# Kernel optimization log

Measured on AMD Instinct MI355X. Metric: run time of the kernel, lower is better.

Reference implementation:

```python
import jax, jax.numpy as jnp
import numpy as np

B = 1
S = 256          # sequence_size (pair repr is S x S)
C = 128          # channel_size_pair
NHEAD = 4
HID = 32         # hidden_channel
SCALE = 1.0 / float(np.sqrt(HID))
EPS = 1e-5


def setup_inputs() -> dict:
    key = jax.random.key(0)
    ks = jax.random.split(key, 9)
    init = 0.02
    return {
        "pair_repr": jax.random.normal(ks[0], (B, S, S, C), dtype=jnp.float32),
        "gamma": jnp.ones((C,), dtype=jnp.float32),
        "beta": jnp.zeros((C,), dtype=jnp.float32),
        "Wq": jax.random.normal(ks[1], (C, NHEAD * HID), dtype=jnp.float32) * init,
        "Wk": jax.random.normal(ks[2], (C, NHEAD * HID), dtype=jnp.float32) * init,
        "Wv": jax.random.normal(ks[3], (C, NHEAD * HID), dtype=jnp.float32) * init,
        "Wb": jax.random.normal(ks[4], (C, NHEAD), dtype=jnp.float32) * init,
        "Wg": jax.random.normal(ks[5], (C, NHEAD * HID), dtype=jnp.float32) * init,
        "bg": jnp.zeros((NHEAD * HID,), dtype=jnp.float32),
        "Wo": jax.random.normal(ks[6], (NHEAD * HID, C), dtype=jnp.float32) * init,
        "bo": jnp.zeros((C,), dtype=jnp.float32),
    }


def _to_heads(t):
    # [b, h, w, n*d] -> [b, n, h, w, d]
    b, h, w, _ = t.shape
    return t.reshape(b, h, w, NHEAD, HID).transpose(0, 3, 1, 2, 4)


def reference(pair_repr, gamma, beta, Wq, Wk, Wv, Wb, Wg, bg, Wo, bo):
    # LayerNorm over channel dim
    mu = jnp.mean(pair_repr, axis=-1, keepdims=True)
    var = jnp.var(pair_repr, axis=-1, keepdims=True)
    z = (pair_repr - mu) * jax.lax.rsqrt(var + EPS) * gamma + beta

    q = _to_heads(z @ Wq)  # [b, n, i, j, d]
    k = _to_heads(z @ Wk)
    v = _to_heads(z @ Wv)
    g = _to_heads(jax.nn.sigmoid(z @ Wg + bg))

    # bias: [b, h, w, n] -> [b, n, h, w]; 'ending' broadcasts it over the j axis
    bias = (z @ Wb).transpose(0, 3, 1, 2)

    # 'ending' branch: attend over the row index k for each column j
    dots = SCALE * jnp.einsum('bnijd,bnkjd->bnijk', q, k) + bias[:, :, :, None, :]
    attn = jax.nn.softmax(dots, axis=4)
    out = g * jnp.einsum('bnijk,bnkjd->bnijd', attn, v)

    # [b, n, i, j, d] -> [b, i, j, n*d]
    out = out.transpose(0, 2, 3, 1, 4).reshape(B, S, S, NHEAD * HID)
    return out @ Wo + bo
```

## Files before the change

kernel.cpp:

```cpp
#include <hip/hip_runtime.h>
#include <hip/hip_bf16.h>
#include <math.h>

#define SCALE 0.1767766952966369f
#define LN_EPS 1e-5f

typedef short bf16x8 __attribute__((ext_vector_type(8)));
typedef float f32x4 __attribute__((ext_vector_type(4)));

__device__ __forceinline__ unsigned short f2bf(float f) {
    __hip_bfloat16 h = __float2bfloat16(f);
    return *reinterpret_cast<unsigned short*>(&h);
}
__device__ __forceinline__ float bf2f(unsigned short u) {
    union { unsigned int u32; float f; } c;
    c.u32 = ((unsigned int)u) << 16;
    return c.f;
}
__device__ __forceinline__ unsigned int pack2(float a, float b) {
    return (unsigned int)f2bf(a) | ((unsigned int)f2bf(b) << 16);
}

__global__ __launch_bounds__(256)
void k_prep(const float* __restrict__ Wq, const float* __restrict__ Wk,
            const float* __restrict__ Wv, const float* __restrict__ Wg,
            const float* __restrict__ Wo, const float* __restrict__ Wb,
            unsigned short* __restrict__ WT, unsigned short* __restrict__ WbT)
{
    if (blockIdx.x == 20) {
        int t = threadIdx.x;
        int row = t >> 4, k0 = (t & 15) * 8;
        unsigned int u[4];
        #pragma unroll
        for (int e = 0; e < 4; ++e) {
            float a = 0.f, b = 0.f;
            if (row < 4) {
                a = Wb[(k0 + 2*e    )*4 + row];
                b = Wb[(k0 + 2*e + 1)*4 + row];
            }
            u[e] = pack2(a, b);
        }
        *(uint4*)(WbT + row*128 + k0) = make_uint4(u[0], u[1], u[2], u[3]);
        return;
    }
    int idx = blockIdx.x * 256 + threadIdx.x;
    int m   = idx >> 10;
    int col = (idx >> 3) & 127;
    int k0  = (idx & 7) * 16;
    const float* W = (m==0) ? Wq : (m==1) ? Wk : (m==2) ? Wv : (m==3) ? Wg : Wo;
    unsigned int u[8];
    #pragma unroll
    for (int e = 0; e < 8; ++e) {
        float a = W[(k0 + 2*e    )*128 + col];
        float b = W[(k0 + 2*e + 1)*128 + col];
        u[e] = pack2(a, b);
    }
    uint4* dst = (uint4*)(WT + m*16384 + col*128 + k0);
    dst[0] = make_uint4(u[0], u[1], u[2], u[3]);
    dst[1] = make_uint4(u[4], u[5], u[6], u[7]);
}

__global__ __launch_bounds__(256)
void k_ln_proj(const float* __restrict__ x, const float* __restrict__ gamma,
               const float* __restrict__ beta,
               const unsigned short* __restrict__ WT,
               const unsigned short* __restrict__ WbT,
               const float* __restrict__ bg,
               unsigned short* __restrict__ Q, unsigned short* __restrict__ K,
               unsigned short* __restrict__ VT, unsigned short* __restrict__ G,
               float* __restrict__ BIAS)
{
    __shared__ unsigned short Wbuf[64*136];
    __shared__ unsigned short stg[4][2176];

    const int t    = threadIdx.x;
    const int lane = t & 63, w = t >> 6;
    const int l15  = lane & 15, quad = lane >> 4;
    const int j    = blockIdx.x >> 2;
    const int ti   = (blockIdx.x & 3) * 64 + w*16;
    unsigned short* sw = stg[w];

    float v[32];
    {
        const float* xr = x + ((size_t)(ti + l15)*256 + j)*128;
        float sum = 0.f, ssq = 0.f;
        #pragma unroll
        for (int kt = 0; kt < 4; ++kt) {
            float4 f0 = *(const float4*)(xr + kt*32 + quad*8);
            float4 f1 = *(const float4*)(xr + kt*32 + quad*8 + 4);
            v[kt*8+0]=f0.x; v[kt*8+1]=f0.y; v[kt*8+2]=f0.z; v[kt*8+3]=f0.w;
            v[kt*8+4]=f1.x; v[kt*8+5]=f1.y; v[kt*8+6]=f1.z; v[kt*8+7]=f1.w;
            sum += f0.x+f0.y+f0.z+f0.w + f1.x+f1.y+f1.z+f1.w;
            ssq += f0.x*f0.x+f0.y*f0.y+f0.z*f0.z+f0.w*f0.w
                 + f1.x*f1.x+f1.y*f1.y+f1.z*f1.z+f1.w*f1.w;
        }
        sum += __shfl_xor(sum, 16); ssq += __shfl_xor(ssq, 16);
        sum += __shfl_xor(sum, 32); ssq += __shfl_xor(ssq, 32);
        float mu  = sum * (1.f/128.f);
        float var = ssq * (1.f/128.f) - mu*mu;
        float rs  = rsqrtf(var + LN_EPS);
        #pragma unroll
        for (int kt = 0; kt < 4; ++kt)
            #pragma unroll
            for (int e = 0; e < 8; ++e) {
                int c = kt*32 + quad*8 + e;
                v[kt*8+e] = (v[kt*8+e]-mu)*rs*gamma[c] + beta[c];
            }
    }
    bf16x8 afrag[4];
    #pragma unroll
    for (int kt = 0; kt < 4; ++kt)
        #pragma unroll
        for (int e = 0; e < 8; ++e)
            afrag[kt][e] = (short)f2bf(v[kt*8+e]);

    {
        f32x4 bacc = (f32x4){0.f,0.f,0.f,0.f};
        #pragma unroll
        for (int kt = 0; kt < 4; ++kt) {
            bf16x8 b = *(const bf16x8*)(WbT + (size_t)l15*128 + kt*32 + quad*8);
            bacc = __builtin_amdgcn_mfma_f32_16x16x32_bf16(afrag[kt], b, bacc, 0, 0, 0);
        }
        if (l15 < 4) {
            #pragma unroll
            for (int reg = 0; reg < 4; ++reg)
                BIAS[l15*65536 + ((ti >> 2) + quad)*1024 + j*4 + reg] = bacc[reg];
        }
    }

    #pragma unroll 1
    for (int mm = 0; mm < 4; ++mm) {
        f32x4 acc[8];
        #pragma unroll
        for (int nt = 0; nt < 8; ++nt) acc[nt] = (f32x4){0.f,0.f,0.f,0.f};

        #pragma unroll 1
        for (int half = 0; half < 2; ++half) {
            __syncthreads();
            #pragma unroll
            for (int r = 0; r < 4; ++r) {
                int idx = r*256 + t;
                int col = idx >> 4, kc = idx & 15;
                *(uint4*)&Wbuf[col*136 + kc*8] =
                    *(const uint4*)&WT[mm*16384 + (half*64 + col)*128 + kc*8];
            }
            __syncthreads();

            #pragma unroll
            for (int kt = 0; kt < 4; ++kt) {
                #pragma unroll
                for (int nt2 = 0; nt2 < 4; ++nt2) {
                    bf16x8 b = *(const bf16x8*)&Wbuf[(nt2*16 + l15)*136 + kt*32 + quad*8];
                    if (mm == 2)
                        acc[half*4 + nt2] = __builtin_amdgcn_mfma_f32_16x16x32_bf16(
                            b, afrag[kt], acc[half*4 + nt2], 0, 0, 0);
                    else
                        acc[half*4 + nt2] = __builtin_amdgcn_mfma_f32_16x16x32_bf16(
                            afrag[kt], b, acc[half*4 + nt2], 0, 0, 0);
                }
            }
        }

        if (mm == 2) {
            #pragma unroll
            for (int nt = 0; nt < 8; ++nt)
                #pragma unroll
                for (int reg = 0; reg < 4; ++reg)
                    sw[(nt*16 + quad*4 + reg)*16 + l15] = f2bf(acc[nt][reg]);
            #pragma unroll
            for (int it = 0; it < 4; ++it) {
                int idx = it*64 + lane;
                int ch = idx >> 1, c = idx & 1;
                uint4 val = *(const uint4*)&sw[ch*16 + c*8];
                int nh = ch >> 5, d = ch & 31;
                *(uint4*)&VT[(((size_t)(nh*256 + j))*32 + d)*256 + ti + c*8] = val;
            }
        } else {
            #pragma unroll
            for (int nt = 0; nt < 8; ++nt) {
                int cc = nt*16 + l15;
                float bgv = (mm == 3) ? bg[cc] : 0.f;
                #pragma unroll
                for (int reg = 0; reg < 4; ++reg) {
                    float val = acc[nt][reg];
                    if (mm == 0)      val *= SCALE;
                    else if (mm == 3) val = 1.f/(1.f + __expf(-(val + bgv)));
                    sw[(quad*4 + reg)*136 + cc] = f2bf(val);
                }
            }
            {
                int row = lane >> 2, c = lane & 3;
                unsigned short* Dst = (mm == 0) ? Q : (mm == 1) ? K : G;
                #pragma unroll
                for (int nh = 0; nh < 4; ++nh) {
                    uint4 val = *(const uint4*)&sw[row*136 + nh*32 + c*8];
                    *(uint4*)&Dst[(((size_t)(nh*256 + j))*256 + ti + row)*32 + c*8] = val;
                }
            }
        }
    }
}

__global__ __launch_bounds__(256)
void k_attn(const unsigned short* __restrict__ Q, const unsigned short* __restrict__ K,
            const unsigned short* __restrict__ VT, const unsigned short* __restrict__ G,
            const float* __restrict__ BIAS, unsigned short* __restrict__ AO)
{
    __shared__ unsigned short P_lds[4][16*264];

    const int t    = threadIdx.x;
    const int n    = blockIdx.x >> 10;
    const int j    = (blockIdx.x >> 2) & 255;
    const int ic   = blockIdx.x & 3;
    const int lane = t & 63, w = t >> 6;
    const int l15  = lane & 15, quad = lane >> 4;
    const int i0   = ic*64 + w*16;

    const size_t nb = (size_t)(n*256 + j);
    const unsigned short* qb  = Q  + nb*8192;
    const unsigned short* kb  = K  + nb*8192;
    const unsigned short* vtb = VT + nb*8192;
    const unsigned short* gb  = G  + nb*8192;
    const float* biasn = BIAS + n*65536;
    unsigned short* Pw = P_lds[w];

    bf16x8 a = *(const bf16x8*)(qb + (size_t)(i0 + l15)*32 + quad*8);
    f32x4 acc[16];
    #pragma unroll
    for (int kt = 0; kt < 16; ++kt) {
        bf16x8 b = *(const bf16x8*)(kb + (size_t)(kt*16 + l15)*32 + quad*8);
        acc[kt] = __builtin_amdgcn_mfma_f32_16x16x32_bf16(a, b, (f32x4){0.f,0.f,0.f,0.f}, 0, 0, 0);
    }

    float mx[4] = {-1e30f, -1e30f, -1e30f, -1e30f};
    #pragma unroll
    for (int kt = 0; kt < 16; ++kt) {
        float4 bv = *(const float4*)&biasn[((i0 >> 2) + quad)*1024 + (kt*16 + l15)*4];
        acc[kt][0] += bv.x; acc[kt][1] += bv.y;
        acc[kt][2] += bv.z; acc[kt][3] += bv.w;
        #pragma unroll
        for (int reg = 0; reg < 4; ++reg)
            mx[reg] = fmaxf(mx[reg], acc[kt][reg]);
    }
    #pragma unroll
    for (int m = 1; m <= 8; m <<= 1) {
        #pragma unroll
        for (int reg = 0; reg < 4; ++reg)
            mx[reg] = fmaxf(mx[reg], __shfl_xor(mx[reg], m));
    }

    float sm[4] = {0.f, 0.f, 0.f, 0.f};
    #pragma unroll
    for (int kt = 0; kt < 16; ++kt) {
        #pragma unroll
        for (int reg = 0; reg < 4; ++reg) {
            float e = __expf(acc[kt][reg] - mx[reg]);
            acc[kt][reg] = e;
            sm[reg] += e;
        }
    }
    #pragma unroll
    for (int m = 1; m <= 8; m <<= 1) {
        #pragma unroll
        for (int reg = 0; reg < 4; ++reg)
            sm[reg] += __shfl_xor(sm[reg], m);
    }
    float rinv[4];
    #pragma unroll
    for (int reg = 0; reg < 4; ++reg) rinv[reg] = 1.f / sm[reg];

    #pragma unroll
    for (int kt = 0; kt < 16; ++kt) {
        #pragma unroll
        for (int reg = 0; reg < 4; ++reg)
            Pw[(quad*4 + reg)*264 + kt*16 + l15] = f2bf(acc[kt][reg]);
    }

    f32x4 o[2];
    o[0] = (f32x4){0.f,0.f,0.f,0.f};
    o[1] = (f32x4){0.f,0.f,0.f,0.f};
    #pragma unroll
    for (int kt8 = 0; kt8 < 8; ++kt8) {
        bf16x8 pa = *(const bf16x8*)(Pw + l15*264 + kt8*32 + quad*8);
        #pragma unroll
        for (int nt = 0; nt < 2; ++nt) {
            bf16x8 vb = *(const bf16x8*)(vtb + (size_t)(nt*16 + l15)*256 + kt8*32 + quad*8);
            o[nt] = __builtin_amdgcn_mfma_f32_16x16x32_bf16(pa, vb, o[nt], 0, 0, 0);
        }
    }

    #pragma unroll
    for (int nt = 0; nt < 2; ++nt) {
        #pragma unroll
        for (int reg = 0; reg < 4; ++reg) {
            int i = i0 + quad*4 + reg;
            float g = bf2f(gb[(size_t)i*32 + nt*16 + l15]);
            float res = o[nt][reg] * rinv[reg] * g;
            Pw[(quad*4 + reg)*40 + nt*16 + l15] = f2bf(res);
        }
    }
    {
        int row = lane >> 2, oo = lane & 3;
        uint4 val = *(const uint4*)&Pw[row*40 + oo*8];
        *(uint4*)&AO[((size_t)((i0 + row)*256 + j))*128 + n*32 + oo*8] = val;
    }
}

__global__ __launch_bounds__(256)
void k_out(const unsigned short* __restrict__ AO, const unsigned short* __restrict__ WOT,
           const float* __restrict__ bo, float* __restrict__ out)
{
    __shared__ unsigned short WB[128*136];

    const int t    = threadIdx.x;
    const int lane = t & 63, w = t >> 6;
    const int l15  = lane & 15, quad = lane >> 4;
    const int p0   = (blockIdx.x*4 + w) * 16;

    #pragma unroll
    for (int r = 0; r < 8; ++r) {
        int idx = r*256 + t;
        int col = idx >> 4, kc = idx & 15;
        *(uint4*)&WB[col*136 + kc*8] = *(const uint4*)&WOT[col*128 + kc*8];
    }

    bf16x8 a[4];
    #pragma unroll
    for (int kt = 0; kt < 4; ++kt)
        a[kt] = *(const bf16x8*)(AO + (size_t)(p0 + l15)*128 + kt*32 + quad*8);

    __syncthreads();

    f32x4 acc[8];
    #pragma unroll
    for (int nt = 0; nt < 8; ++nt) acc[nt] = (f32x4){0.f,0.f,0.f,0.f};
    #pragma unroll
    for (int kt = 0; kt < 4; ++kt) {
        #pragma unroll
        for (int nt = 0; nt < 8; ++nt) {
            bf16x8 b = *(const bf16x8*)&WB[(nt*16 + l15)*136 + kt*32 + quad*8];
            acc[nt] = __builtin_amdgcn_mfma_f32_16x16x32_bf16(a[kt], b, acc[nt], 0, 0, 0);
        }
    }
    #pragma unroll
    for (int nt = 0; nt < 8; ++nt) {
        float bov = bo[nt*16 + l15];
        #pragma unroll
        for (int reg = 0; reg < 4; ++reg) {
            int p = p0 + quad*4 + reg;
            out[(size_t)p*128 + nt*16 + l15] = acc[nt][reg] + bov;
        }
    }
}

extern "C" void kernel_launch(void* const* d_in, const int* in_sizes, int n_in,
                              void* d_out, int out_size, void* d_ws, size_t ws_size,
                              hipStream_t stream) {
    (void)in_sizes; (void)n_in; (void)out_size; (void)ws_size;
    const float* x     = (const float*)d_in[0];
    const float* gamma = (const float*)d_in[1];
    const float* beta  = (const float*)d_in[2];
    const float* Wq    = (const float*)d_in[3];
    const float* Wk    = (const float*)d_in[4];
    const float* Wv    = (const float*)d_in[5];
    const float* Wb    = (const float*)d_in[6];
    const float* Wg    = (const float*)d_in[7];
    const float* bg    = (const float*)d_in[8];
    const float* Wo    = (const float*)d_in[9];
    const float* bo    = (const float*)d_in[10];
    float* out = (float*)d_out;

    unsigned short* WT  = (unsigned short*)d_ws;
    unsigned short* WbT = WT + 5*16384;
    unsigned short* Qp  = WbT + 2048;
    unsigned short* Kp  = Qp + 8388608;
    unsigned short* VTp = Kp + 8388608;
    unsigned short* Gp  = VTp + 8388608;
    float* Bp   = (float*)(Gp + 8388608);
    unsigned short* AOp = (unsigned short*)(Bp + 262144);
    unsigned short* WOT = WT + 4*16384;

    k_prep<<<21, 256, 0, stream>>>(Wq, Wk, Wv, Wg, Wo, Wb, WT, WbT);
    k_ln_proj<<<1024, 256, 0, stream>>>(x, gamma, beta, WT, WbT, bg,
                                        Qp, Kp, VTp, Gp, Bp);
    k_attn<<<4096, 256, 0, stream>>>(Qp, Kp, VTp, Gp, Bp, AOp);
    k_out<<<1024, 256, 0, stream>>>(AOp, WOT, bo, out);
}
```

Measured before the change: 209.0 us.

## Prefetch weight tiles into registers and process all rows per attention block

In the LN+projection kernel, the next weight tile is loaded from global memory into registers while the current tile's MFMAs run, so global latency overlaps compute instead of sitting between the barriers. Gamma and beta are read as float4 vectors. The attention kernel now gives each block a whole (head, column) pair, with each wave looping over four 16-row tiles, so K/V/bias reads are shared within a block and the grid is four times smaller. The risk is lower parallelism and occupancy in attention, plus extra register pressure from the prefetch buffer.

After: 233.2 us. 1.12x slower.

```diff
diff --git a/kernel.cpp b/kernel.cpp
--- a/kernel.cpp
+++ b/kernel.cpp
@@ -80,6 +80,14 @@
     const int ti   = (blockIdx.x & 3) * 64 + w*16;
     unsigned short* sw = stg[w];
 
+    const int kc8 = (t & 15) * 8;
+    const int cb  = t >> 4;
+
+    uint4 pre[4];
+    #pragma unroll
+    for (int r = 0; r < 4; ++r)
+        pre[r] = *(const uint4*)&WT[cb*128 + r*2048 + kc8];
+
     float v[32];
     {
         const float* xr = x + ((size_t)(ti + l15)*256 + j)*128;
@@ -100,12 +108,20 @@
         float var = ssq * (1.f/128.f) - mu*mu;
         float rs  = rsqrtf(var + LN_EPS);
         #pragma unroll
-        for (int kt = 0; kt < 4; ++kt)
-            #pragma unroll
-            for (int e = 0; e < 8; ++e) {
-                int c = kt*32 + quad*8 + e;
-                v[kt*8+e] = (v[kt*8+e]-mu)*rs*gamma[c] + beta[c];
-            }
+        for (int kt = 0; kt < 4; ++kt) {
+            float4 g0 = *(const float4*)&gamma[kt*32 + quad*8];
+            float4 g1 = *(const float4*)&gamma[kt*32 + quad*8 + 4];
+            float4 b0 = *(const float4*)&beta [kt*32 + quad*8];
+            float4 b1 = *(const float4*)&beta [kt*32 + quad*8 + 4];
+            v[kt*8+0] = (v[kt*8+0]-mu)*rs*g0.x + b0.x;
+            v[kt*8+1] = (v[kt*8+1]-mu)*rs*g0.y + b0.y;
+            v[kt*8+2] = (v[kt*8+2]-mu)*rs*g0.z + b0.z;
+            v[kt*8+3] = (v[kt*8+3]-mu)*rs*g0.w + b0.w;
+            v[kt*8+4] = (v[kt*8+4]-mu)*rs*g1.x + b1.x;
+            v[kt*8+5] = (v[kt*8+5]-mu)*rs*g1.y + b1.y;
+            v[kt*8+6] = (v[kt*8+6]-mu)*rs*g1.z + b1.z;
+            v[kt*8+7] = (v[kt*8+7]-mu)*rs*g1.w + b1.w;
+        }
     }
     bf16x8 afrag[4];
     #pragma unroll
@@ -138,13 +154,20 @@
         for (int half = 0; half < 2; ++half) {
             __syncthreads();
             #pragma unroll
-            for (int r = 0; r < 4; ++r) {
-                int idx = r*256 + t;
-                int col = idx >> 4, kc = idx & 15;
-                *(uint4*)&Wbuf[col*136 + kc*8] =
-                    *(const uint4*)&WT[mm*16384 + (half*64 + col)*128 + kc*8];
-            }
+            for (int r = 0; r < 4; ++r)
+                *(uint4*)&Wbuf[(cb + r*16)*136 + kc8] = pre[r];
             __syncthreads();
+
+            {
+                int p = mm*2 + half;
+                if (p < 7) {
+                    int nm = (p + 1) >> 1, nh = (p + 1) & 1;
+                    #pragma unroll
+                    for (int r = 0; r < 4; ++r)
+                        pre[r] = *(const uint4*)&WT[nm*16384 + nh*8192
+                                                    + cb*128 + r*2048 + kc8];
+                }
+            }
 
             #pragma unroll
             for (int kt = 0; kt < 4; ++kt) {
@@ -209,12 +232,10 @@
     __shared__ unsigned short P_lds[4][16*264];
 
     const int t    = threadIdx.x;
-    const int n    = blockIdx.x >> 10;
-    const int j    = (blockIdx.x >> 2) & 255;
-    const int ic   = blockIdx.x & 3;
+    const int n    = blockIdx.x >> 8;
+    const int j    = blockIdx.x & 255;
     const int lane = t & 63, w = t >> 6;
     const int l15  = lane & 15, quad = lane >> 4;
-    const int i0   = ic*64 + w*16;
 
     const size_t nb = (size_t)(n*256 + j);
     const unsigned short* qb  = Q  + nb*8192;
@@ -224,85 +245,90 @@
     const float* biasn = BIAS + n*65536;
     unsigned short* Pw = P_lds[w];
 
-    bf16x8 a = *(const bf16x8*)(qb + (size_t)(i0 + l15)*32 + quad*8);
-    f32x4 acc[16];
-    #pragma unroll
-    for (int kt = 0; kt < 16; ++kt) {
-        bf16x8 b = *(const bf16x8*)(kb + (size_t)(kt*16 + l15)*32 + quad*8);
-        acc[kt] = __builtin_amdgcn_mfma_f32_16x16x32_bf16(a, b, (f32x4){0.f,0.f,0.f,0.f}, 0, 0, 0);
-    }
-
-    float mx[4] = {-1e30f, -1e30f, -1e30f, -1e30f};
-    #pragma unroll
-    for (int kt = 0; kt < 16; ++kt) {
-        float4 bv = *(const float4*)&biasn[((i0 >> 2) + quad)*1024 + (kt*16 + l15)*4];
-        acc[kt][0] += bv.x; acc[kt][1] += bv.y;
-        acc[kt][2] += bv.z; acc[kt][3] += bv.w;
-        #pragma unroll
-        for (int reg = 0; reg < 4; ++reg)
-            mx[reg] = fmaxf(mx[reg], acc[kt][reg]);
-    }
-    #pragma unroll
-    for (int m = 1; m <= 8; m <<= 1) {
-        #pragma unroll
-        for (int reg = 0; reg < 4; ++reg)
-            mx[reg] = fmaxf(mx[reg], __shfl_xor(mx[reg], m));
-    }
-
-    float sm[4] = {0.f, 0.f, 0.f, 0.f};
-    #pragma unroll
-    for (int kt = 0; kt < 16; ++kt) {
-        #pragma unroll
-        for (int reg = 0; reg < 4; ++reg) {
-            float e = __expf(acc[kt][reg] - mx[reg]);
-            acc[kt][reg] = e;
-            sm[reg] += e;
-        }
-    }
-    #pragma unroll
-    for (int m = 1; m <= 8; m <<= 1) {
-        #pragma unroll
-        for (int reg = 0; reg < 4; ++reg)
-            sm[reg] += __shfl_xor(sm[reg], m);
-    }
-    float rinv[4];
-    #pragma unroll
-    for (int reg = 0; reg < 4; ++reg) rinv[reg] = 1.f / sm[reg];
-
-    #pragma unroll
-    for (int kt = 0; kt < 16; ++kt) {
-        #pragma unroll
-        for (int reg = 0; reg < 4; ++reg)
-            Pw[(quad*4 + reg)*264 + kt*16 + l15] = f2bf(acc[kt][reg]);
-    }
-
-    f32x4 o[2];
-    o[0] = (f32x4){0.f,0.f,0.f,0.f};
-    o[1] = (f32x4){0.f,0.f,0.f,0.f};
-    #pragma unroll
-    for (int kt8 = 0; kt8 < 8; ++kt8) {
-        bf16x8 pa = *(const bf16x8*)(Pw + l15*264 + kt8*32 + quad*8);
+    #pragma unroll 1
+    for (int tt = 0; tt < 4; ++tt) {
+        const int i0 = w*64 + tt*16;
+
+        bf16x8 a = *(const bf16x8*)(qb + (size_t)(i0 + l15)*32 + quad*8);
+        f32x4 acc[16];
+        #pragma unroll
+        for (int kt = 0; kt < 16; ++kt) {
+            bf16x8 b = *(const bf16x8*)(kb + (size_t)(kt*16 + l15)*32 + quad*8);
+            acc[kt] = __builtin_amdgcn_mfma_f32_16x16x32_bf16(a, b, (f32x4){0.f,0.f,0.f,0.f}, 0, 0, 0);
+        }
+
+        float mx[4] = {-1e30f, -1e30f, -1e30f, -1e30f};
+        #pragma unroll
+        for (int kt = 0; kt < 16; ++kt) {
+            float4 bv = *(const float4*)&biasn[((i0 >> 2) + quad)*1024 + (kt*16 + l15)*4];
+            acc[kt][0] += bv.x; acc[kt][1] += bv.y;
+            acc[kt][2] += bv.z; acc[kt][3] += bv.w;
+            #pragma unroll
+            for (int reg = 0; reg < 4; ++reg)
+                mx[reg] = fmaxf(mx[reg], acc[kt][reg]);
+        }
+        #pragma unroll
+        for (int m = 1; m <= 8; m <<= 1) {
+            #pragma unroll
+            for (int reg = 0; reg < 4; ++reg)
+                mx[reg] = fmaxf(mx[reg], __shfl_xor(mx[reg], m));
+        }
+
+        float sm[4] = {0.f, 0.f, 0.f, 0.f};
+        #pragma unroll
+        for (int kt = 0; kt < 16; ++kt) {
+            #pragma unroll
+            for (int reg = 0; reg < 4; ++reg) {
+                float e = __expf(acc[kt][reg] - mx[reg]);
+                acc[kt][reg] = e;
+                sm[reg] += e;
+            }
+        }
+        #pragma unroll
+        for (int m = 1; m <= 8; m <<= 1) {
+            #pragma unroll
+            for (int reg = 0; reg < 4; ++reg)
+                sm[reg] += __shfl_xor(sm[reg], m);
+        }
+        float rinv[4];
+        #pragma unroll
+        for (int reg = 0; reg < 4; ++reg) rinv[reg] = 1.f / sm[reg];
+
+        #pragma unroll
+        for (int kt = 0; kt < 16; ++kt) {
+            #pragma unroll
+            for (int reg = 0; reg < 4; ++reg)
+                Pw[(quad*4 + reg)*264 + kt*16 + l15] = f2bf(acc[kt][reg]);
+        }
+
+        f32x4 o[2];
+        o[0] = (f32x4){0.f,0.f,0.f,0.f};
+        o[1] = (f32x4){0.f,0.f,0.f,0.f};
+        #pragma unroll
+        for (int kt8 = 0; kt8 < 8; ++kt8) {
+            bf16x8 pa = *(const bf16x8*)(Pw + l15*264 + kt8*32 + quad*8);
+            #pragma unroll
+            for (int nt = 0; nt < 2; ++nt) {
+                bf16x8 vb = *(const bf16x8*)(vtb + (size_t)(nt*16 + l15)*256 + kt8*32 + quad*8);
+                o[nt] = __builtin_amdgcn_mfma_f32_16x16x32_bf16(pa, vb, o[nt], 0, 0, 0);
+            }
+        }
+
         #pragma unroll
         for (int nt = 0; nt < 2; ++nt) {
-            bf16x8 vb = *(const bf16x8*)(vtb + (size_t)(nt*16 + l15)*256 + kt8*32 + quad*8);
-            o[nt] = __builtin_amdgcn_mfma_f32_16x16x32_bf16(pa, vb, o[nt], 0, 0, 0);
-        }
-    }
-
-    #pragma unroll
-    for (int nt = 0; nt < 2; ++nt) {
-        #pragma unroll
-        for (int reg = 0; reg < 4; ++reg) {
-            int i = i0 + quad*4 + reg;
-            float g = bf2f(gb[(size_t)i*32 + nt*16 + l15]);
-            float res = o[nt][reg] * rinv[reg] * g;
-            Pw[(quad*4 + reg)*40 + nt*16 + l15] = f2bf(res);
-        }
-    }
-    {
-        int row = lane >> 2, oo = lane & 3;
-        uint4 val = *(const uint4*)&Pw[row*40 + oo*8];
-        *(uint4*)&AO[((size_t)((i0 + row)*256 + j))*128 + n*32 + oo*8] = val;
+            #pragma unroll
+            for (int reg = 0; reg < 4; ++reg) {
+                int i = i0 + quad*4 + reg;
+                float g = bf2f(gb[(size_t)i*32 + nt*16 + l15]);
+                float res = o[nt][reg] * rinv[reg] * g;
+                Pw[(quad*4 + reg)*40 + nt*16 + l15] = f2bf(res);
+            }
+        }
+        {
+            int row = lane >> 2, oo = lane & 3;
+            uint4 val = *(const uint4*)&Pw[row*40 + oo*8];
+            *(uint4*)&AO[((size_t)((i0 + row)*256 + j))*128 + n*32 + oo*8] = val;
+        }
     }
 }
 
@@ -383,6 +409,6 @@
     k_prep<<<21, 256, 0, stream>>>(Wq, Wk, Wv, Wg, Wo, Wb, WT, WbT);
     k_ln_proj<<<1024, 256, 0, stream>>>(x, gamma, beta, WT, WbT, bg,
                                         Qp, Kp, VTp, Gp, Bp);
-    k_attn<<<4096, 256, 0, stream>>>(Qp, Kp, VTp, Gp, Bp, AOp);
+    k_attn<<<1024, 256, 0, stream>>>(Qp, Kp, VTp, Gp, Bp, AOp);
     k_out<<<1024, 256, 0, stream>>>(AOp, WOT, bo, out);
 }
```
